# Performance work log

Measured on AMD Instinct MI355X. Metric: run time of the kernel, lower is better.

Reference implementation:

```python
import jax, jax.numpy as jnp
import numpy as np

B, C, T = 16, 129, 2000
NF, ED, K = 40, 64, 16

def setup_inputs() -> dict:
    key = jax.random.key(0)
    ks = iter(jax.random.split(key, 48))
    def n(shape, s=0.05):
        return jax.random.normal(next(ks), shape, jnp.float32) * s
    inp = {
        'x': jax.random.normal(next(ks), (B, C, T), jnp.float32),
        # temporal conv (1,25) pad (0,12) + BN (inference running stats)
        'tconv_w': n((NF, 1, 1, 25)), 'tconv_b': jnp.zeros((NF,)),
        'tbn_g': jnp.ones((NF,)), 'tbn_b': jnp.zeros((NF,)), 'tbn_m': n((NF,)), 'tbn_v': jnp.ones((NF,)),
        # spatial conv (C,1) + BN
        'sconv_w': n((NF, NF, C, 1)), 'sconv_b': jnp.zeros((NF,)),
        'sbn_g': jnp.ones((NF,)), 'sbn_b': jnp.zeros((NF,)), 'sbn_m': n((NF,)), 'sbn_v': jnp.ones((NF,)),
        # separable: depthwise (1,15) pad (0,7), pointwise 1x1 -> 2*NF, BN
        'dw_w': n((NF, 1, 1, 15)), 'dw_b': jnp.zeros((NF,)),
        'pw_w': n((2 * NF, NF, 1, 1)), 'pw_b': jnp.zeros((2 * NF,)),
        'pbn_g': jnp.ones((2 * NF,)), 'pbn_b': jnp.zeros((2 * NF,)), 'pbn_m': n((2 * NF,)), 'pbn_v': jnp.ones((2 * NF,)),
        # projection 2*NF -> ED
        'proj_w': n((ED, 2 * NF)), 'proj_b': jnp.zeros((ED,)),
        # ENN cell 0 (input ED)
        'wx0': n((K, ED)), 'L0': jnp.eye(K, dtype=jnp.float32) + 0.1 * n((K, K), 1.0),
        'll0': jnp.asarray(np.log(0.1), jnp.float32), 'b0': jnp.zeros((K,)),
        'ln0_g': jnp.ones((K,)), 'ln0_b': jnp.zeros((K,)),
        # ENN cell 1 (input K)
        'wx1': n((K, K)), 'L1': jnp.eye(K, dtype=jnp.float32) + 0.1 * n((K, K), 1.0),
        'll1': jnp.asarray(np.log(0.1), jnp.float32), 'b1': jnp.zeros((K,)),
        'ln1_g': jnp.ones((K,)), 'ln1_b': jnp.zeros((K,)),
        # collapse
        'wq_w': n((K, K)), 'wq_b': jnp.zeros((K,)), 'log_temp': jnp.asarray(0.0, jnp.float32),
    }
    return inp

def _conv(x, w, b, pad, groups=1):
    y = jax.lax.conv_general_dilated(
        x, w, window_strides=(1, 1), padding=pad,
        dimension_numbers=('NCHW', 'OIHW', 'NCHW'), feature_group_count=groups)
    return y + b[None, :, None, None]

def _bn(x, g, b, m, v, eps=1e-5):
    inv = g / jnp.sqrt(v + eps)
    return x * inv[None, :, None, None] + (b - m * inv)[None, :, None, None]

def _cell(x, h, Wx, L, ll, b, g, be, eps=1e-5):
    E = L @ L.T  # PSD entanglement matrix [K,K]
    pre = x @ Wx.T + h @ E.T - jnp.exp(ll) * h + b
    mu = pre.mean(-1, keepdims=True)
    var = pre.var(-1, keepdims=True)
    pre = (pre - mu) / jnp.sqrt(var + eps) * g + be
    return jnp.tanh(pre)

def _forward(x, tconv_w, tconv_b, tbn_g, tbn_b, tbn_m, tbn_v,
             sconv_w, sconv_b, sbn_g, sbn_b, sbn_m, sbn_v,
             dw_w, dw_b, pw_w, pw_b, pbn_g, pbn_b, pbn_m, pbn_v,
             proj_w, proj_b,
             wx0, L0, ll0, b0, ln0_g, ln0_b,
             wx1, L1, ll1, b1, ln1_g, ln1_b,
             wq_w, wq_b, log_temp):
    # ---- SpatialCNN front-end (BN in inference mode, dropout=identity) ----
    o = x[:, None, :, :]                                        # [B,1,C,T]
    o = _conv(o, tconv_w, tconv_b, ((0, 0), (12, 12)))          # [B,NF,C,T]
    o = jax.nn.elu(_bn(o, tbn_g, tbn_b, tbn_m, tbn_v))
    o = _conv(o, sconv_w, sconv_b, ((0, 0), (0, 0)))            # [B,NF,1,T]
    o = jax.nn.elu(_bn(o, sbn_g, sbn_b, sbn_m, sbn_v))
    o = _conv(o, dw_w, dw_b, ((0, 0), (7, 7)), groups=NF)       # depthwise
    o = _conv(o, pw_w, pw_b, ((0, 0), (0, 0)))                  # [B,2NF,1,T]
    o = jax.nn.elu(_bn(o, pbn_g, pbn_b, pbn_m, pbn_v))
    Bn, Ch, _, Tt = o.shape
    o = o.reshape(Bn, Ch, Tt // 4, 4).mean(-1)                  # AvgPool (1,4) -> [B,2NF,T']
    feats = o.transpose(0, 2, 1) @ proj_w.T + proj_b            # [B,T',ED]
    # ---- Entangled RNN over T' steps (lax.scan) ----
    h_init = (jnp.zeros((Bn, K), feats.dtype), jnp.zeros((Bn, K), feats.dtype))
    def step(carry, xt):
        h0, h1 = carry
        h0 = _cell(xt, h0, wx0, L0, ll0, b0, ln0_g, ln0_b)
        h1 = _cell(h0, h1, wx1, L1, ll1, b1, ln1_g, ln1_b)
        return (h0, h1), None
    (h0, h1), _ = jax.lax.scan(step, h_init, feats.transpose(1, 0, 2))
    Z = h1                                                       # [B,K]
    # ---- Collapse attention ----
    q = Z @ wq_w.T + wq_b
    scores = jnp.sum(q * Z, axis=-1, keepdims=True)              # [B,1]
    alpha = jax.nn.softmax(scores / jnp.exp(log_temp), axis=-1)  # [B,1]
    return Z, alpha

def reference(x, tconv_w, tconv_b, tbn_g, tbn_b, tbn_m, tbn_v,
              sconv_w, sconv_b, sbn_g, sbn_b, sbn_m, sbn_v,
              dw_w, dw_b, pw_w, pw_b, pbn_g, pbn_b, pbn_m, pbn_v,
              proj_w, proj_b,
              wx0, L0, ll0, b0, ln0_g, ln0_b,
              wx1, L1, ll1, b1, ln1_g, ln1_b,
              wq_w, wq_b, log_temp):
    return _forward(x, tconv_w, tconv_b, tbn_g, tbn_b, tbn_m, tbn_v,
                    sconv_w, sconv_b, sbn_g, sbn_b, sbn_m, sbn_v,
                    dw_w, dw_b, pw_w, pw_b, pbn_g, pbn_b, pbn_m, pbn_v,
                    proj_w, proj_b,
                    wx0, L0, ll0, b0, ln0_g, ln0_b,
                    wx1, L1, ll1, b1, ln1_g, ln1_b,
                    wq_w, wq_b, log_temp)
```

## Files before the change

### kernel.cpp

```cpp
#include <hip/hip_runtime.h>
#include <math.h>

#define B_ 16
#define C_ 129
#define T_ 2000
#define NF_ 40
#define ED_ 64
#define K_ 16
#define TP_ 500

#define OFF_SB2 1040
#define OFF_PWC 1088
#define OFF_PB2 4288
#define OFF_WP  4368
#define OFF_BP  5648
#define OFF_M0  5664
#define OFF_M1  5920
#define OFF_W1A 6224
#define OFF_W2U 8192
#define OFF_XP  1495040
#define OFF_S2R 1623040

typedef __attribute__((ext_vector_type(8))) short s8v;
typedef __attribute__((ext_vector_type(4))) float f4v;
typedef __attribute__((ext_vector_type(4))) __fp16 h4v;
typedef __attribute__((ext_vector_type(2))) __fp16 h2v;

#define XROW 292

__device__ __forceinline__ float elu_f(float x) {
    return x > 0.f ? x : (__expf(x) - 1.f);
}
__device__ __forceinline__ unsigned bfr(float v) {
    return (__float_as_uint(v) + 0x8000u) >> 16;
}


#define MFMA16(a, b, c) __builtin_amdgcn_mfma_f32_16x16x16f16(a, b, c, 0, 0, 0)

#define EXP2F(x) __builtin_amdgcn_exp2f(x)
#define RSQF(x) __builtin_amdgcn_rsqf(x)

__device__ __forceinline__ void split4(f4v v, h4v& hi, h4v& lo) {
    union UH { h4v h4; h2v h2[2]; } H, L;
    H.h2[0] = __builtin_amdgcn_cvt_pkrtz(v[0], v[1]);
    H.h2[1] = __builtin_amdgcn_cvt_pkrtz(v[2], v[3]);
    L.h2[0] = __builtin_amdgcn_cvt_pkrtz(v[0] - (float)H.h2[0][0],
                                         v[1] - (float)H.h2[0][1]);
    L.h2[1] = __builtin_amdgcn_cvt_pkrtz(v[2] - (float)H.h2[1][0],
                                         v[3] - (float)H.h2[1][1]);
    hi = H.h4;
    lo = L.h4;
}

union U4 { struct { h4v hi, lo; } s; uint4 u; };

struct P0 {
    const float *tconv_w, *tconv_b, *tbn_g, *tbn_b, *tbn_m, *tbn_v;
    const float *sconv_b, *sbn_g, *sbn_b, *sbn_m, *sbn_v;
    const float *pw_w, *pw_b, *pbn_g, *pbn_b, *pbn_m, *pbn_v;
    const float *proj_w, *proj_b, *wx0, *b0, *L0, *ll0, *L1, *ll1;
    const float *sconv_w;
    float* ws;
};

__global__ __launch_bounds__(256) void k0_all(P0 p) {
    const int tid = threadIdx.x;
    float* ws = p.ws;
    const float eps = 1e-5f;

    if (blockIdx.x < 1250) {
        const int i = blockIdx.x * 256 + tid;
        if (i < 320000)
            ((float4*)(ws + OFF_S2R))[i] = make_float4(0.f, 0.f, 0.f, 0.f);
        return;
    }
    if (blockIdx.x < 1444) {
        const int e = (blockIdx.x - 1250) * 256 + tid;
        if (e >= C_ * 3 * 2 * 64) return;
        unsigned short* w2b = (unsigned short*)(ws + OFF_W2U);
        const int c = e / 384;
        int r = e - c * 384;
        const int mt = r >> 7; r &= 127;
        const int kc = r >> 6;
        const int lane = r & 63;
        const int g = mt * 16 + (lane & 15);
        const float sinv = (g < NF_) ? p.sbn_g[g] * rsqrtf(p.sbn_v[g] + 1e-5f) : 0.f;
        unsigned short o[8];
#pragma unroll
        for (int j = 0; j < 8; ++j) {
            const int f = kc * 32 + (lane >> 4) * 8 + j;
            float v = 0.f;
            if (g < NF_ && f < NF_) v = p.sconv_w[g * (NF_ * C_) + f * C_ + c] * sinv;
            o[j] = (unsigned short)bfr(v);
        }
        unsigned short* dst = w2b + (size_t)e * 8;
#pragma unroll
        for (int j = 0; j < 8; ++j) dst[j] = o[j];
        return;
    }

    const int gtid = (blockIdx.x - 1444) * 256 + tid;
    const int stride = 8 * 256;
    for (int e = gtid; e < 192; e += stride) {
        const int mt = e >> 6, L = e & 63;
        const int f = mt * 16 + (L & 15);
        float inv = 0.f, bias = 0.f;
        if (f < NF_) {
            inv = p.tbn_g[f] / sqrtf(p.tbn_v[f] + eps);
            bias = p.tconv_b[f] * inv + p.tbn_b[f] - p.tbn_m[f] * inv;
        }
        unsigned short* dst = ((unsigned short*)(ws + OFF_W1A)) + e * 8;
#pragma unroll
        for (int j = 0; j < 8; ++j) {
            const int k = (L >> 4) * 8 + j;
            float v = 0.f;
            if (f < NF_) {
                if (k < 25) v = p.tconv_w[f * 25 + k] * inv;
                else if (k == 25) v = bias;
            }
            dst[j] = (unsigned short)bfr(v);
        }
    }
    for (int f = gtid; f < NF_; f += stride) {
        const float sinv = p.sbn_g[f] / sqrtf(p.sbn_v[f] + eps);
        ws[OFF_SB2 + f] = p.sconv_b[f] * sinv + p.sbn_b[f] - p.sbn_m[f] * sinv;
    }
    for (int e = gtid; e < 3200; e += stride) {
        const int g = e / 40;
        const float pinv = p.pbn_g[g] / sqrtf(p.pbn_v[g] + eps);
        ws[OFF_PWC + e] = p.pw_w[e] * pinv;
    }
    for (int g = gtid; g < 80; g += stride) {
        const float pinv = p.pbn_g[g] / sqrtf(p.pbn_v[g] + eps);
        ws[OFF_PB2 + g] = p.pw_b[g] * pinv + p.pbn_b[g] - p.pbn_m[g] * pinv;
    }
    for (int e = gtid; e < 1280; e += stride) {
        const int k = e / 80, g = e - k * 80;
        float a = 0.f;
        for (int ee = 0; ee < ED_; ++ee)
            a = fmaf(p.wx0[k * ED_ + ee], p.proj_w[ee * 80 + g], a);
        ws[OFF_WP + e] = a;
    }
    for (int k = gtid; k < K_; k += stride) {
        float a = p.b0[k];
        for (int ee = 0; ee < ED_; ++ee)
            a = fmaf(p.wx0[k * ED_ + ee], p.proj_b[ee], a);
        ws[OFF_BP + k] = a;
    }
    for (int e = gtid; e < 256; e += stride) {
        const int k = e >> 4, j = e & 15;
        float a0 = 0.f, a1 = 0.f;
        for (int i = 0; i < 16; ++i) {
            a0 = fmaf(p.L0[k * 16 + i], p.L0[j * 16 + i], a0);
            a1 = fmaf(p.L1[k * 16 + i], p.L1[j * 16 + i], a1);
        }
        if (k == j) { a0 -= expf(p.ll0[0]); a1 -= expf(p.ll1[0]); }
        ws[OFF_M0 + e] = a0;
        ws[OFF_M1 + e] = a1;
    }
}

__global__ __launch_bounds__(256, 4) void k1_mfma(
    const float* __restrict__ x, const unsigned short* __restrict__ w1a,
    const unsigned short* __restrict__ w2b, float* __restrict__ s2raw) {
    __shared__ float xs[17 * XROW];
    __shared__ unsigned int vsI[2048];

    const int tid = threadIdx.x;
    const int split = blockIdx.x & 7;
    const int tile = (blockIdx.x >> 3) & 7;
    const int b = blockIdx.x >> 6;
    const int c0 = (split * C_) >> 3;
    const int c1 = ((split + 1) * C_) >> 3;
    const int cc = c1 - c0;
    const int t0 = tile << 8;
    const int w = tid >> 6;
    const int lane = tid & 63;
    const int n = lane & 15;
    const int q = lane >> 4;
    const int qh = q >> 1;
    const int q1_2 = (q & 1) * 2;
    const bool q3 = (q == 3);
    const int wb = w << 9;
    const int w64 = w << 6;
    const int ln8 = n + q * 8;

    for (int i = tid; i < 2048; i += 256) vsI[i] = 0u;
    for (int e = tid; e < cc * XROW; e += 256) {
        const int cl = e / XROW;
        const int i = e - cl * XROW;
        const int t = t0 - 12 + i;
        float v = 0.f;
        if ((unsigned)t < (unsigned)T_) v = x[(b * C_ + c0 + cl) * T_ + t];
        xs[e] = v;
    }
    __syncthreads();

    const s8v* w1a8 = (const s8v*)w1a;
    s8v wA[3];
#pragma unroll
    for (int mt = 0; mt < 3; ++mt) wA[mt] = w1a8[mt * 64 + lane];

    f4v acc[4][3];
#pragma unroll
    for (int nt = 0; nt < 4; ++nt)
#pragma unroll
        for (int mt = 0; mt < 3; ++mt) acc[nt][mt] = (f4v)0.f;

    const s8v* w2b8 = (const s8v*)w2b;
    const f4v z4 = (f4v)0.f;

    for (int cl = 0; cl < cc; ++cl) {
        const int c = c0 + cl;
        s8v af[3][2];
#pragma unroll
        for (int mt = 0; mt < 3; ++mt)
#pragma unroll
            for (int kc = 0; kc < 2; ++kc)
                af[mt][kc] = w2b8[((c * 3 + mt) * 2 + kc) * 64 + lane];

        const float* xrow = &xs[cl * XROW + w64 + ln8];

#pragma unroll
        for (int nt = 0; nt < 4; ++nt) {
            float bx[8];
#pragma unroll
            for (int j = 0; j < 8; ++j) bx[j] = xrow[nt * 16 + j];
            if (q3) bx[1] = 1.0f;
            unsigned pw_[4];
#pragma unroll
            for (int jj = 0; jj < 4; ++jj)
                pw_[jj] = bfr(bx[2 * jj]) |
                    ((__float_as_uint(bx[2 * jj + 1]) + 0x8000u) & 0xFFFF0000u);
            const s8v bh = *(const s8v*)pw_;
#pragma unroll
            for (int mt = 0; mt < 3; ++mt) {
                const f4v vT = __builtin_amdgcn_mfma_f32_16x16x32_bf16(
                    wA[mt], bh, z4, 0, 0, 0);
                const float e0 = elu_f(vT[0]);
                const float e1 = elu_f(vT[1]);
                const float e2 = elu_f(vT[2]);
                const float e3 = elu_f(vT[3]);
                const unsigned lo = bfr(e0) |
                    ((__float_as_uint(e1) + 0x8000u) & 0xFFFF0000u);
                const unsigned hi = bfr(e2) |
                    ((__float_as_uint(e3) + 0x8000u) & 0xFFFF0000u);
                const int base = wb + ((2 * mt + qh) << 6) + (n << 2) + q1_2;
                vsI[base] = lo;
                vsI[base + 1] = hi;
            }
            __builtin_amdgcn_wave_barrier();
            const s8v b0 = *(const s8v*)&vsI[wb + (q << 6) + (n << 2)];
            const s8v b1 = *(const s8v*)&vsI[wb + ((4 + q) << 6) + (n << 2)];
#pragma unroll
            for (int mt = 0; mt < 3; ++mt) {
                acc[nt][mt] = __builtin_amdgcn_mfma_f32_16x16x32_bf16(
                    af[mt][0], b0, acc[nt][mt], 0, 0, 0);
                acc[nt][mt] = __builtin_amdgcn_mfma_f32_16x16x32_bf16(
                    af[mt][1], b1, acc[nt][mt], 0, 0, 0);
            }
            __builtin_amdgcn_wave_barrier();
        }
    }

#pragma unroll
    for (int nt = 0; nt < 4; ++nt) {
        const int t = t0 + w * 64 + nt * 16 + n;
        if (t >= T_) continue;
#pragma unroll
        for (int mt = 0; mt < 3; ++mt) {
#pragma unroll
            for (int r = 0; r < 4; ++r) {
                const int g = mt * 16 + q * 4 + r;
                if (g < NF_)
                    atomicAdd(&s2raw[(b * NF_ + g) * T_ + t], acc[nt][mt][r]);
            }
        }
    }
}

__global__ __launch_bounds__(256) void k2_dwpw(
    const float* __restrict__ s2raw, const float* __restrict__ sb2,
    const float* __restrict__ dw_w, const float* __restrict__ dw_b,
    const float* __restrict__ pwc, const float* __restrict__ pb2,
    const float* __restrict__ WP, const float* __restrict__ bp,
    float* __restrict__ xp) {
    __shared__ float st[NF_ * 114];
    __shared__ float dwo[NF_ * 100];
    __shared__ float dwwl[NF_ * 15];
    __shared__ float dwbl[NF_];
    __shared__ float pwcl[80 * 40];
    __shared__ float pb2l[80];
    __shared__ float WPl[K_ * 80];
    __shared__ float bpl[K_];
    __shared__ float po[80 * 25];
    const int tid = threadIdx.x;
    const int b = blockIdx.x / 20;
    const int tp0 = (blockIdx.x % 20) * 25;
    const int tbase = tp0 * 4 - 7;
    for (int e = tid; e < NF_ * 114; e += 256) {
        const int f = e / 114;
        const int i = e - f * 114;
        const int t = tbase + i;
        float v = 0.f;
        if ((unsigned)t < (unsigned)T_)
            v = elu_f(s2raw[(b * NF_ + f) * T_ + t] + sb2[f]);
        st[e] = v;
    }
    for (int e = tid; e < 600; e += 256) dwwl[e] = dw_w[e];
    for (int e = tid; e < 3200; e += 256) pwcl[e] = pwc[e];
    for (int e = tid; e < 1280; e += 256) WPl[e] = WP[e];
    if (tid < NF_) dwbl[tid] = dw_b[tid];
    if (tid < 80) pb2l[tid] = pb2[tid];
    if (tid < K_) bpl[tid] = bp[tid];
    __syncthreads();
    for (int e = tid; e < 4000; e += 256) {
        const int f = e / 100;
        const int tq = e - f * 100;
        float a = dwbl[f];
#pragma unroll
        for (int kk = 0; kk < 15; ++kk)
            a = fmaf(dwwl[f * 15 + kk], st[f * 114 + tq + kk], a);
        dwo[e] = a;
    }
    __syncthreads();
    for (int e = tid; e < 2000; e += 256) {
        const int g = e / 25;
        const int tp = e - g * 25;
        float sum = 0.f;
#pragma unroll
        for (int dt = 0; dt < 4; ++dt) {
            float a = pb2l[g];
            for (int f = 0; f < NF_; ++f)
                a = fmaf(pwcl[g * 40 + f], dwo[f * 100 + tp * 4 + dt], a);
            sum += elu_f(a);
        }
        po[e] = sum * 0.25f;
    }
    __syncthreads();
    for (int e = tid; e < 400; e += 256) {
        const int tp = e >> 4;
        const int k = e & 15;
        float a = bpl[k];
        for (int g = 0; g < 80; ++g)
            a = fmaf(WPl[k * 80 + g], po[g * 25 + tp], a);
        xp[(tp0 + tp) * 256 + ((k & 12) << 4) + (b << 2) + (k & 3)] = a;
    }
}

__global__ __launch_bounds__(128, 1) void k3_scan(
    const float* __restrict__ xp, const float* __restrict__ M0,
    const float* __restrict__ M1, const float* __restrict__ wx1,
    const float* __restrict__ b1, const float* __restrict__ ln0_g,
    const float* __restrict__ ln0_b, const float* __restrict__ ln1_g,
    const float* __restrict__ ln1_b, float* __restrict__ out) {
    __shared__ uint4 hbuf[2][64];
    const int tid = threadIdx.x;
    const int w = tid >> 6;
    const int lane = tid & 63;
    const int n = lane & 15;
    const int q = lane >> 4;
    const int r0 = q << 2;
    const f4v z4 = (f4v)0.f;
    const float C2 = 2.8853900817779268f;

    h4v Ahi{}, Alo{}, Whi{}, Wlo{};
    f4v G, Bb, B1C = z4;
    if (w == 0) {
        const f4v a = *(const f4v*)(M0 + n * 16 + r0);
        split4(a, Ahi, Alo);
#pragma unroll
        for (int j = 0; j < 4; ++j) {
            G[j] = C2 * ln0_g[r0 + j];
            Bb[j] = C2 * ln0_b[r0 + j];
        }
    } else {
        const f4v a = *(const f4v*)(M1 + n * 16 + r0);
        split4(a, Ahi, Alo);
        const f4v ww = *(const f4v*)(wx1 + n * 16 + r0);
        split4(ww, Whi, Wlo);
        B1C = *(const f4v*)(b1 + r0);
#pragma unroll
        for (int j = 0; j < 4; ++j) {
            G[j] = C2 * ln1_g[r0 + j];
            Bb[j] = C2 * ln1_b[r0 + j];
        }
    }

    h4v Shi{}, Slo{};
    f4v hlast = z4;
    const f4v* xp4 = (const f4v*)xp;
    f4v Xb0 = z4, Xb1 = z4;
    if (w == 0) {
        Xb0 = xp4[lane];
        Xb1 = xp4[64 + lane];
    }

    for (int t = 0; t <= TP_; ++t) {
        __syncthreads();
        f4v pre;
        bool act;
        if (w == 0) {
            act = (t < TP_);
            if (act) {
                const f4v Xc = Xb0;
                Xb0 = Xb1;
                int tn = t + 2;
                if (tn > TP_ - 1) tn = TP_ - 1;
                Xb1 = xp4[tn * 64 + lane];
                f4v c1 = MFMA16(Ahi, Shi, Xc);
                f4v c2 = MFMA16(Ahi, Slo, z4);
                c2 = MFMA16(Alo, Shi, c2);
                pre = c1 + c2;
            }
        } else {
            act = (t > 0);
            if (act) {
                U4 R;
                R.u = hbuf[(t - 1) & 1][lane];
                f4v c1 = MFMA16(Whi, R.s.hi, B1C);
                c1 = MFMA16(Wlo, R.s.hi, c1);
                f4v c2 = MFMA16(Ahi, Shi, z4);
                c2 = MFMA16(Alo, Shi, c2);
                f4v c3 = MFMA16(Whi, R.s.lo, z4);
                c3 = MFMA16(Ahi, Slo, c3);
                pre = (c1 + c2) + c3;
            }
        }
        if (act) {
            float s1 = (pre[0] + pre[1]) + (pre[2] + pre[3]);
            float s2 = fmaf(pre[3], pre[3], fmaf(pre[2], pre[2],
                        fmaf(pre[1], pre[1], pre[0] * pre[0])));
            s1 += __shfl_xor(s1, 16);
            s2 += __shfl_xor(s2, 16);
            s1 += __shfl_xor(s1, 32);
            s2 += __shfl_xor(s2, 32);
            const float mu = s1 * 0.0625f;
            const float inv = RSQF(fmaf(s2, 0.0625f, -mu * mu) + 1e-5f);
            f4v hnew;
#pragma unroll
            for (int j = 0; j < 4; ++j) {
                const float coef = inv * G[j];
                const float a2 = fmaf(pre[j], coef, fmaf(-mu, coef, Bb[j]));
                const float e2 = EXP2F(a2);
                hnew[j] = fmaf(-2.f, __builtin_amdgcn_rcpf(e2 + 1.f), 1.f);
            }
            split4(hnew, Shi, Slo);
            if (w == 0) {
                U4 P;
                P.s.hi = Shi;
                P.s.lo = Slo;
                hbuf[t & 1][lane] = P.u;
            } else {
                hlast = hnew;
            }
        }
    }
    if (w == 1) {
        *(f4v*)(out + n * K_ + r0) = hlast;
        if (q == 0) out[256 + n] = 1.0f;
    }
}

extern "C" void kernel_launch(void* const* d_in, const int* in_sizes, int n_in,
                              void* d_out, int out_size, void* d_ws, size_t ws_size,
                              hipStream_t stream) {
    const float* x       = (const float*)d_in[0];
    const float* dw_w    = (const float*)d_in[13];
    const float* dw_b    = (const float*)d_in[14];
    const float* wx1     = (const float*)d_in[29];
    const float* b1      = (const float*)d_in[32];
    const float* ln0_g   = (const float*)d_in[27];
    const float* ln0_b   = (const float*)d_in[28];
    const float* ln1_g   = (const float*)d_in[33];
    const float* ln1_b   = (const float*)d_in[34];
    float* ws = (float*)d_ws;
    float* out = (float*)d_out;

    P0 p;
    p.tconv_w = (const float*)d_in[1]; p.tconv_b = (const float*)d_in[2];
    p.tbn_g = (const float*)d_in[3]; p.tbn_b = (const float*)d_in[4];
    p.tbn_m = (const float*)d_in[5]; p.tbn_v = (const float*)d_in[6];
    p.sconv_b = (const float*)d_in[8];
    p.sbn_g = (const float*)d_in[9]; p.sbn_b = (const float*)d_in[10];
    p.sbn_m = (const float*)d_in[11]; p.sbn_v = (const float*)d_in[12];
    p.pw_w = (const float*)d_in[15]; p.pw_b = (const float*)d_in[16];
    p.pbn_g = (const float*)d_in[17]; p.pbn_b = (const float*)d_in[18];
    p.pbn_m = (const float*)d_in[19]; p.pbn_v = (const float*)d_in[20];
    p.proj_w = (const float*)d_in[21]; p.proj_b = (const float*)d_in[22];
    p.wx0 = (const float*)d_in[23]; p.b0 = (const float*)d_in[26];
    p.L0 = (const float*)d_in[24]; p.ll0 = (const float*)d_in[25];
    p.L1 = (const float*)d_in[30]; p.ll1 = (const float*)d_in[31];
    p.sconv_w = (const float*)d_in[7];
    p.ws = ws;

    unsigned short* w2b = (unsigned short*)(ws + OFF_W2U);
    unsigned short* w1a = (unsigned short*)(ws + OFF_W1A);

    k0_all<<<dim3(1452), dim3(256), 0, stream>>>(p);
    k1_mfma<<<dim3(1024), dim3(256), 0, stream>>>(x, w1a, w2b, ws + OFF_S2R);
    k2_dwpw<<<dim3(320), dim3(256), 0, stream>>>(ws + OFF_S2R, ws + OFF_SB2,
                                                 dw_w, dw_b, ws + OFF_PWC,
                                                 ws + OFF_PB2, ws + OFF_WP, ws + OFF_BP,
                                                 ws + OFF_XP);
    k3_scan<<<dim3(1), dim3(128), 0, stream>>>(ws + OFF_XP, ws + OFF_M0, ws + OFF_M1,
                                               wx1, b1, ln0_g, ln0_b, ln1_g, ln1_b, out);
}
```

Measured before the change: 446.1 us.

## Merge two-wave pipelined scan into single wave without LDS or barriers

The sequential recurrence kernel previously ran cell 0 and cell 1 on two separate waves, passing hidden state through LDS with a __syncthreads every step. It now runs both cells in one 64-lane wave, keeping cell 0's previous state in registers and issuing both cells' MFMAs back to back. This removes the per-step barrier and LDS round trip, and lets the two cells' independent work interleave. The LayerNorm reduction also changes from a sequential two-step butterfly to three parallel shuffles. The cost is more serial work per step on a single wave.

After: 608.1 us. 1.36x slower.

```diff
diff --git a/kernel.cpp b/kernel.cpp
--- a/kernel.cpp
+++ b/kernel.cpp
@@ -53,7 +53,30 @@
     lo = L.h4;
 }
 
-union U4 { struct { h4v hi, lo; } s; uint4 u; };
+__device__ __forceinline__ f4v lnTanh(f4v pre, f4v G, f4v Bb) {
+    float s1 = (pre[0] + pre[1]) + (pre[2] + pre[3]);
+    float s2 = fmaf(pre[1], pre[1], pre[0] * pre[0]) +
+               fmaf(pre[3], pre[3], pre[2] * pre[2]);
+    const float s1a = __shfl_xor(s1, 16);
+    const float s1b = __shfl_xor(s1, 32);
+    const float s1c = __shfl_xor(s1, 48);
+    const float s2a = __shfl_xor(s2, 16);
+    const float s2b = __shfl_xor(s2, 32);
+    const float s2c = __shfl_xor(s2, 48);
+    s1 = (s1 + s1a) + (s1b + s1c);
+    s2 = (s2 + s2a) + (s2b + s2c);
+    const float mu = s1 * 0.0625f;
+    const float inv = RSQF(fmaf(s2, 0.0625f, -mu * mu) + 1e-5f);
+    f4v h;
+#pragma unroll
+    for (int j = 0; j < 4; ++j) {
+        const float coef = inv * G[j];
+        const float a2 = fmaf(pre[j], coef, fmaf(-mu, coef, Bb[j]));
+        const float e2 = EXP2F(a2);
+        h[j] = fmaf(-2.f, __builtin_amdgcn_rcpf(e2 + 1.f), 1.f);
+    }
+    return h;
+}
 
 struct P0 {
     const float *tconv_w, *tconv_b, *tbn_g, *tbn_b, *tbn_m, *tbn_v;
@@ -349,118 +372,82 @@
     }
 }
 
-__global__ __launch_bounds__(128, 1) void k3_scan(
+__global__ __launch_bounds__(64, 1) void k3_scan(
     const float* __restrict__ xp, const float* __restrict__ M0,
     const float* __restrict__ M1, const float* __restrict__ wx1,
     const float* __restrict__ b1, const float* __restrict__ ln0_g,
     const float* __restrict__ ln0_b, const float* __restrict__ ln1_g,
     const float* __restrict__ ln1_b, float* __restrict__ out) {
-    __shared__ uint4 hbuf[2][64];
-    const int tid = threadIdx.x;
-    const int w = tid >> 6;
-    const int lane = tid & 63;
+    const int lane = threadIdx.x;
     const int n = lane & 15;
     const int q = lane >> 4;
     const int r0 = q << 2;
     const f4v z4 = (f4v)0.f;
     const float C2 = 2.8853900817779268f;
 
-    h4v Ahi{}, Alo{}, Whi{}, Wlo{};
-    f4v G, Bb, B1C = z4;
-    if (w == 0) {
-        const f4v a = *(const f4v*)(M0 + n * 16 + r0);
-        split4(a, Ahi, Alo);
-#pragma unroll
-        for (int j = 0; j < 4; ++j) {
-            G[j] = C2 * ln0_g[r0 + j];
-            Bb[j] = C2 * ln0_b[r0 + j];
-        }
-    } else {
-        const f4v a = *(const f4v*)(M1 + n * 16 + r0);
-        split4(a, Ahi, Alo);
-        const f4v ww = *(const f4v*)(wx1 + n * 16 + r0);
-        split4(ww, Whi, Wlo);
-        B1C = *(const f4v*)(b1 + r0);
-#pragma unroll
-        for (int j = 0; j < 4; ++j) {
-            G[j] = C2 * ln1_g[r0 + j];
-            Bb[j] = C2 * ln1_b[r0 + j];
-        }
-    }
-
-    h4v Shi{}, Slo{};
-    f4v hlast = z4;
+    h4v A0hi, A0lo, A1hi, A1lo, Whi, Wlo;
+    { const f4v a = *(const f4v*)(M0 + n * 16 + r0);  split4(a, A0hi, A0lo); }
+    { const f4v a = *(const f4v*)(M1 + n * 16 + r0);  split4(a, A1hi, A1lo); }
+    { const f4v a = *(const f4v*)(wx1 + n * 16 + r0); split4(a, Whi, Wlo); }
+    const f4v B1C = *(const f4v*)(b1 + r0);
+    f4v G0, B0v, G1, B1v;
+#pragma unroll
+    for (int j = 0; j < 4; ++j) {
+        G0[j] = C2 * ln0_g[r0 + j];  B0v[j] = C2 * ln0_b[r0 + j];
+        G1[j] = C2 * ln1_g[r0 + j];  B1v[j] = C2 * ln1_b[r0 + j];
+    }
+
     const f4v* xp4 = (const f4v*)xp;
-    f4v Xb0 = z4, Xb1 = z4;
-    if (w == 0) {
-        Xb0 = xp4[lane];
-        Xb1 = xp4[64 + lane];
-    }
-
-    for (int t = 0; t <= TP_; ++t) {
-        __syncthreads();
-        f4v pre;
-        bool act;
-        if (w == 0) {
-            act = (t < TP_);
-            if (act) {
-                const f4v Xc = Xb0;
-                Xb0 = Xb1;
-                int tn = t + 2;
-                if (tn > TP_ - 1) tn = TP_ - 1;
-                Xb1 = xp4[tn * 64 + lane];
-                f4v c1 = MFMA16(Ahi, Shi, Xc);
-                f4v c2 = MFMA16(Ahi, Slo, z4);
-                c2 = MFMA16(Alo, Shi, c2);
-                pre = c1 + c2;
-            }
-        } else {
-            act = (t > 0);
-            if (act) {
-                U4 R;
-                R.u = hbuf[(t - 1) & 1][lane];
-                f4v c1 = MFMA16(Whi, R.s.hi, B1C);
-                c1 = MFMA16(Wlo, R.s.hi, c1);
-                f4v c2 = MFMA16(Ahi, Shi, z4);
-                c2 = MFMA16(Alo, Shi, c2);
-                f4v c3 = MFMA16(Whi, R.s.lo, z4);
-                c3 = MFMA16(Ahi, Slo, c3);
-                pre = (c1 + c2) + c3;
-            }
-        }
-        if (act) {
-            float s1 = (pre[0] + pre[1]) + (pre[2] + pre[3]);
-            float s2 = fmaf(pre[3], pre[3], fmaf(pre[2], pre[2],
-                        fmaf(pre[1], pre[1], pre[0] * pre[0])));
-            s1 += __shfl_xor(s1, 16);
-            s2 += __shfl_xor(s2, 16);
-            s1 += __shfl_xor(s1, 32);
-            s2 += __shfl_xor(s2, 32);
-            const float mu = s1 * 0.0625f;
-            const float inv = RSQF(fmaf(s2, 0.0625f, -mu * mu) + 1e-5f);
-            f4v hnew;
-#pragma unroll
-            for (int j = 0; j < 4; ++j) {
-                const float coef = inv * G[j];
-                const float a2 = fmaf(pre[j], coef, fmaf(-mu, coef, Bb[j]));
-                const float e2 = EXP2F(a2);
-                hnew[j] = fmaf(-2.f, __builtin_amdgcn_rcpf(e2 + 1.f), 1.f);
-            }
-            split4(hnew, Shi, Slo);
-            if (w == 0) {
-                U4 P;
-                P.s.hi = Shi;
-                P.s.lo = Slo;
-                hbuf[t & 1][lane] = P.u;
-            } else {
-                hlast = hnew;
-            }
-        }
-    }
-    if (w == 1) {
-        *(f4v*)(out + n * K_ + r0) = hlast;
-        if (q == 0) out[256 + n] = 1.0f;
-    }
+    f4v Xb0 = xp4[lane];
+    f4v Xb1 = xp4[64 + lane];
+
+    h4v S0hi, S0lo, S1hi{}, S1lo{};
+
+    {
+        const f4v h0 = lnTanh(Xb0, G0, B0v);
+        split4(h0, S0hi, S0lo);
+        Xb0 = Xb1;
+        Xb1 = xp4[2 * 64 + lane];
+    }
+
+    for (int t = 1; t < TP_; ++t) {
+        const h4v P0hi = S0hi, P0lo = S0lo;
+        const f4v Xc = Xb0;
+        Xb0 = Xb1;
+        const int tn = (t + 2 < TP_) ? t + 2 : TP_ - 1;
+        Xb1 = xp4[tn * 64 + lane];
+
+        f4v c1 = MFMA16(A0hi, S0hi, Xc);
+        f4v c2 = MFMA16(A0hi, S0lo, z4);
+        c2 = MFMA16(A0lo, S0hi, c2);
+        f4v d1 = MFMA16(Whi, P0hi, B1C);
+        d1 = MFMA16(A1hi, S1hi, d1);
+        f4v d2 = MFMA16(Wlo, P0hi, z4);
+        d2 = MFMA16(A1hi, S1lo, d2);
+        f4v d3 = MFMA16(Whi, P0lo, z4);
+        d3 = MFMA16(A1lo, S1hi, d3);
+
+        const f4v pre0 = c1 + c2;
+        const f4v pre1 = (d1 + d2) + d3;
+        const f4v h0 = lnTanh(pre0, G0, B0v);
+        const f4v h1 = lnTanh(pre1, G1, B1v);
+        split4(h0, S0hi, S0lo);
+        split4(h1, S1hi, S1lo);
+    }
+
+    f4v hlast;
+    {
+        f4v d1 = MFMA16(Whi, S0hi, B1C);
+        d1 = MFMA16(A1hi, S1hi, d1);
+        f4v d2 = MFMA16(Wlo, S0hi, z4);
+        d2 = MFMA16(A1hi, S1lo, d2);
+        f4v d3 = MFMA16(Whi, S0lo, z4);
+        d3 = MFMA16(A1lo, S1hi, d3);
+        hlast = lnTanh((d1 + d2) + d3, G1, B1v);
+    }
+
+    *(f4v*)(out + n * K_ + r0) = hlast;
+    if (q == 0) out[256 + n] = 1.0f;
 }
 
 extern "C" void kernel_launch(void* const* d_in, const int* in_sizes, int n_in,
@@ -504,6 +491,6 @@
                                                  dw_w, dw_b, ws + OFF_PWC,
                                                  ws + OFF_PB2, ws + OFF_WP, ws + OFF_BP,
                                                  ws + OFF_XP);
-    k3_scan<<<dim3(1), dim3(128), 0, stream>>>(ws + OFF_XP, ws + OFF_M0, ws + OFF_M1,
-                                               wx1, b1, ln0_g, ln0_b, ln1_g, ln1_b, out);
-}
+    k3_scan<<<dim3(1), dim3(64), 0, stream>>>(ws + OFF_XP, ws + OFF_M0, ws + OFF_M1,
+                                              wx1, b1, ln0_g, ln0_b, ln1_g, ln1_b, out);
+}
```
